# Optimization experiments

Hardware: AMD Instinct MI355X
Metric: run time of the kernel (lower is better)

## Reference

```python
import jax, jax.numpy as jnp
import numpy as np

DECAY = 0.99
EPS = 1e-05


def setup_inputs() -> dict:
    key = jax.random.key(0)
    k1, k2, k3 = jax.random.split(key, 3)
    N, K, D = 131072, 1024, 64
    return {
        "z": jax.random.normal(k1, (N, D), dtype=jnp.float32),
        "embeddings": jax.random.normal(k2, (K, D), dtype=jnp.float32),
        "cluster_size": jnp.ones((K,), dtype=jnp.float32),
        "ema_embed_sum": jax.random.normal(k3, (K, D), dtype=jnp.float32),
    }


def reference(z, embeddings, cluster_size, ema_embed_sum):
    # z: [N, D]; embeddings/ema_embed_sum: [K, D]; cluster_size: [K]
    N, D = z.shape
    K = embeddings.shape[0]

    # squared pairwise distances via the ||a||^2 - 2ab + ||b||^2 expansion
    d = (
        jnp.sum(z * z, axis=-1, keepdims=True)
        - 2.0 * (z @ embeddings.T)
        + jnp.sum(embeddings * embeddings, axis=-1)
    )  # [N, K]
    encoding_indices = jnp.argmin(d, axis=1)  # [N]
    z_q = embeddings[encoding_indices]  # [N, D]

    # EMA codebook update (training mode; one_hot.sum(0) == counts, one_hot.T @ z == segment_sum)
    counts = jax.ops.segment_sum(jnp.ones((N,), z.dtype), encoding_indices, num_segments=K)
    new_cluster_size = cluster_size * DECAY + (1.0 - DECAY) * counts
    embed_sum = jax.ops.segment_sum(z, encoding_indices, num_segments=K)  # [K, D]
    new_ema_embed_sum = ema_embed_sum * DECAY + (1.0 - DECAY) * embed_sum
    n = jnp.sum(new_cluster_size)
    cs = (new_cluster_size + EPS) / (n + K * EPS) * n
    new_embeddings = new_ema_embed_sum / cs[:, None]

    commitment_loss = jnp.mean((z - z_q) ** 2)
    z_q_st = z + jax.lax.stop_gradient(z_q - z)  # value == z_q
    return (z_q_st, commitment_loss, encoding_indices, new_embeddings, new_cluster_size, new_ema_embed_sum)
```

## Files before the change

kernel.cpp:

```cpp
#include <hip/hip_runtime.h>

#define N_PTS 131072
#define K_CODES 1024
#define DIM 64
#define DECAYF 0.99f
#define OMDF 0.01f
#define EPSF 1e-5f

#define OUT_ZQ      0
#define OUT_LOSS    8388608
#define OUT_IDX     8388609
#define OUT_NEWEMB  8519681
#define OUT_NEWCS   8585217
#define OUT_NEWEMA  8586241

#define WS_C8       0
#define WS_ACNT     8192
#define WS_LOSS     8208
#define WS_EMBSUM   8224
#define WS_ZERO_END 73760
#define WS_ENORM    73760
#define WS_CUR8     74784
#define WS_CS       82976
#define WS_AMBIG    84000
#define WS_ORDER    215072
#define WS_E2       346144

typedef __attribute__((ext_vector_type(8))) short bf16x8;
typedef __attribute__((ext_vector_type(4))) float f32x4;

static __device__ inline short f2bf(float f) {
    unsigned u = __float_as_uint(f);
    unsigned r = (u + 0x7fffu + ((u >> 16) & 1u)) >> 16;
    return (short)r;
}
static __device__ inline float bf2f(short h) {
    return __uint_as_float(((unsigned)(unsigned short)h) << 16);
}

__global__ __launch_bounds__(256) void econv_kernel(const float* __restrict__ E,
                                                    short* __restrict__ E2,
                                                    float* __restrict__ enorm) {
    int k = blockIdx.x * 256 + threadIdx.x;
    const float* ep = E + (size_t)k * DIM;
    short* o = E2 + (size_t)k * 128;
    float s = 0.f;
#pragma unroll
    for (int d = 0; d < 64; ++d) {
        float f = ep[d];
        s += f * f;
        float m = -2.f * f;
        short h = f2bf(m);
        o[d] = h;
        o[64 + d] = f2bf(m - bf2f(h));
    }
    enorm[k] = s;
}

__global__ __launch_bounds__(256) void argmin_mfma(const float* __restrict__ z,
                                                   const short* __restrict__ E2,
                                                   const float* __restrict__ enorm,
                                                   float* __restrict__ out_idx_f,
                                                   float* __restrict__ counts8,
                                                   int* __restrict__ ambig_cnt,
                                                   int* __restrict__ ambig,
                                                   float* __restrict__ loss_ws) {
    int tid = threadIdx.x;
    int w = tid >> 6, lane = tid & 63;
    int c = lane & 15, q = lane >> 4;
    int mbase = blockIdx.x * 256 + w * 64;

    bf16x8 a[4][4];
    float znorm_t[4];
#pragma unroll
    for (int t = 0; t < 4; ++t) {
        const float* zp = z + (size_t)(mbase + t * 16 + c) * DIM;
        const float4* z4a = (const float4*)(zp + q * 8);
        const float4* z4b = (const float4*)(zp + 32 + q * 8);
        float f[16];
        float4 v0 = z4a[0], v1 = z4a[1], v2 = z4b[0], v3 = z4b[1];
        f[0]=v0.x; f[1]=v0.y; f[2]=v0.z; f[3]=v0.w;
        f[4]=v1.x; f[5]=v1.y; f[6]=v1.z; f[7]=v1.w;
        f[8]=v2.x; f[9]=v2.y; f[10]=v2.z; f[11]=v2.w;
        f[12]=v3.x; f[13]=v3.y; f[14]=v3.z; f[15]=v3.w;
        float zn = 0.f;
#pragma unroll
        for (int j = 0; j < 16; ++j) zn += f[j] * f[j];
#pragma unroll
        for (int off = 16; off < 64; off <<= 1) zn += __shfl_xor(zn, off);
        znorm_t[t] = zn;
#pragma unroll
        for (int j = 0; j < 8; ++j) {
            short h0 = f2bf(f[j]);
            a[t][0][j] = h0;
            a[t][2][j] = f2bf(f[j] - bf2f(h0));
            short h1 = f2bf(f[8 + j]);
            a[t][1][j] = h1;
            a[t][3][j] = f2bf(f[8 + j] - bf2f(h1));
        }
    }

    float s1[16], s2[16];
#pragma unroll
    for (int idx = 0; idx < 16; ++idx) { s1[idx] = INFINITY; s2[idx] = INFINITY; }

    unsigned vcode = (unsigned)c;
    for (int tile = 0; tile < 64; ++tile) {
        const bf16x8* bp = (const bf16x8*)E2 + ((size_t)(tile * 16 + c) * 16) + q;
        bf16x8 bh0 = bp[0], bh1 = bp[4], bl0 = bp[8], bl1 = bp[12];
        float en = enorm[tile * 16 + c];
#pragma unroll
        for (int t = 0; t < 4; ++t) {
            f32x4 acc = {en, en, en, en};
            acc = __builtin_amdgcn_mfma_f32_16x16x32_bf16(a[t][0], bl0, acc, 0, 0, 0);
            acc = __builtin_amdgcn_mfma_f32_16x16x32_bf16(a[t][1], bl1, acc, 0, 0, 0);
            acc = __builtin_amdgcn_mfma_f32_16x16x32_bf16(a[t][2], bh0, acc, 0, 0, 0);
            acc = __builtin_amdgcn_mfma_f32_16x16x32_bf16(a[t][3], bh1, acc, 0, 0, 0);
            acc = __builtin_amdgcn_mfma_f32_16x16x32_bf16(a[t][0], bh0, acc, 0, 0, 0);
            acc = __builtin_amdgcn_mfma_f32_16x16x32_bf16(a[t][1], bh1, acc, 0, 0, 0);
#pragma unroll
            for (int i = 0; i < 4; ++i) {
                float sp = __uint_as_float(
                    (__float_as_uint(acc[i]) & 0xFFFFFC00u) | vcode);
                int idx = t * 4 + i;
                float ns2 = __builtin_amdgcn_fmed3f(s1[idx], s2[idx], sp);
                s1[idx] = fminf(s1[idx], sp);
                s2[idx] = ns2;
            }
        }
        vcode += 16;
    }

#pragma unroll
    for (int off = 1; off < 16; off <<= 1) {
#pragma unroll
        for (int idx = 0; idx < 16; ++idx) {
            float os1 = __shfl_xor(s1[idx], off);
            float os2 = __shfl_xor(s2[idx], off);
            float ns1 = fminf(s1[idx], os1);
            s2[idx] = fminf(fmaxf(s1[idx], os1), fminf(s2[idx], os2));
            s1[idx] = ns1;
        }
    }

    float znr[16];
#pragma unroll
    for (int t = 0; t < 4; ++t)
#pragma unroll
        for (int i = 0; i < 4; ++i)
            znr[t * 4 + i] = __shfl(znorm_t[t], (q << 4) | (q * 4 + i), 64);

    __shared__ float lred[16];
    float lsum = 0.f;
    if (c == 0) {
#pragma unroll
        for (int idx = 0; idx < 16; ++idx) {
            int t = idx >> 2, i = idx & 3;
            int row = mbase + t * 16 + q * 4 + i;
            unsigned b1 = __float_as_uint(s1[idx]);
            int code = (int)(b1 & 1023u);
            out_idx_f[row] = (float)code;
            float s1v = __uint_as_float(b1 & 0xFFFFFC00u);
            float gap = s2[idx] - s1[idx];
            float tau = 0.008f + 8e-4f * (fabsf(s1[idx]) + fabsf(s2[idx]));
            if (gap >= tau) {
                atomicAdd(&counts8[(((unsigned)row >> 8) & 7) * K_CODES + code], 1.0f);
                lsum += znr[idx] + s1v;
            } else {
                int p = atomicAdd(ambig_cnt, 1);
                ambig[p] = row;
            }
        }
        lred[w * 4 + q] = lsum;
    }
    __syncthreads();
    if (tid == 0) {
        float tot = 0.f;
#pragma unroll
        for (int i = 0; i < 16; ++i) tot += lred[i];
        atomicAdd(loss_ws, tot);
    }
}

__global__ __launch_bounds__(256) void rescue_kernel(const float* __restrict__ z,
                                                     const float* __restrict__ E,
                                                     const float* __restrict__ enorm,
                                                     const int* __restrict__ ambig_cnt,
                                                     const int* __restrict__ ambig,
                                                     float* __restrict__ out_idx_f,
                                                     float* __restrict__ counts8,
                                                     float* __restrict__ loss_ws) {
    int lane = threadIdx.x & 63;
    int wave = (blockIdx.x * 256 + threadIdx.x) >> 6;
    int nw = gridDim.x * 4;
    int cnt = *ambig_cnt;
    for (int a = 2 * wave; a < cnt; a += 2 * nw) {
        int row0 = ambig[a];
        bool two = (a + 1) < cnt;
        int row1 = two ? ambig[a + 1] : row0;
        const float4* zp0 = (const float4*)(z + (size_t)row0 * DIM);
        const float4* zp1 = (const float4*)(z + (size_t)row1 * DIM);
        float4 zr0[16], zr1[16];
        float zn0 = 0.f, zn1 = 0.f;
#pragma unroll
        for (int i = 0; i < 16; ++i) {
            float4 u = zp0[i], v = zp1[i];
            zr0[i] = u; zr1[i] = v;
            zn0 += u.x * u.x + u.y * u.y + u.z * u.z + u.w * u.w;
            zn1 += v.x * v.x + v.y * v.y + v.z * v.z + v.w * v.w;
        }
        float best0 = INFINITY, best1 = INFINITY;
        int bi0 = 0, bi1 = 0;
        for (int j = 0; j < 16; ++j) {
            int code = j * 64 + lane;
            const float4* ep = (const float4*)(E + (size_t)code * DIM);
            float a0 = 0.f, a1 = 0.f, a2 = 0.f, a3 = 0.f;
            float c0 = 0.f, c1 = 0.f, c2 = 0.f, c3 = 0.f;
#pragma unroll
            for (int i = 0; i < 16; ++i) {
                float4 ev = ep[i];
                a0 += zr0[i].x * ev.x; a1 += zr0[i].y * ev.y;
                a2 += zr0[i].z * ev.z; a3 += zr0[i].w * ev.w;
                c0 += zr1[i].x * ev.x; c1 += zr1[i].y * ev.y;
                c2 += zr1[i].z * ev.z; c3 += zr1[i].w * ev.w;
            }
            float en = enorm[code];
            float s0 = en - 2.f * ((a0 + a1) + (a2 + a3));
            float s1 = en - 2.f * ((c0 + c1) + (c2 + c3));
            if (s0 < best0) { best0 = s0; bi0 = code; }
            if (s1 < best1) { best1 = s1; bi1 = code; }
        }
#pragma unroll
        for (int off = 1; off < 64; off <<= 1) {
            float ob = __shfl_xor(best0, off);
            int oi = __shfl_xor(bi0, off);
            if (ob < best0 || (ob == best0 && oi < bi0)) { best0 = ob; bi0 = oi; }
            float ob1 = __shfl_xor(best1, off);
            int oi1 = __shfl_xor(bi1, off);
            if (ob1 < best1 || (ob1 == best1 && oi1 < bi1)) { best1 = ob1; bi1 = oi1; }
        }
        if (lane == 0) {
            out_idx_f[row0] = (float)bi0;
            atomicAdd(&counts8[(((unsigned)row0 >> 8) & 7) * K_CODES + bi0], 1.0f);
            float ladd = zn0 + best0;
            if (two) {
                out_idx_f[row1] = (float)bi1;
                atomicAdd(&counts8[(((unsigned)row1 >> 8) & 7) * K_CODES + bi1], 1.0f);
                ladd += zn1 + best1;
            }
            atomicAdd(loss_ws, ladd);
        }
    }
}

__global__ __launch_bounds__(256) void zq_write_kernel(const float* __restrict__ E,
                                                       const float* __restrict__ idx_f,
                                                       float* __restrict__ zq) {
    __shared__ int s_k[256];
    int tid = threadIdx.x;
    int rbase = blockIdx.x * 256;
    s_k[tid] = (int)idx_f[rbase + tid];
    __syncthreads();
    size_t ebase = (size_t)rbase * DIM;
#pragma unroll 4
    for (int it = 0; it < 64; ++it) {
        int le = it * 256 + tid;
        int rl = le >> 6, d = le & 63;
        zq[ebase + le] = E[(size_t)s_k[rl] * DIM + d];
    }
}

__global__ __launch_bounds__(1024) void scan_kernel(const float* __restrict__ cluster_size,
                                                    const float* __restrict__ counts8,
                                                    float* __restrict__ ncs_out,
                                                    float* __restrict__ cs_ws,
                                                    int* __restrict__ cursor8) {
    int k = threadIdx.x;
    int lane = k & 63, wv = k >> 6;
    float c8[8];
    float cnt = 0.f;
#pragma unroll
    for (int s = 0; s < 8; ++s) { c8[s] = counts8[s * K_CODES + k]; cnt += c8[s]; }
    float ncs = cluster_size[k] * DECAYF + OMDF * cnt;
    ncs_out[k] = ncs;

    int v = (int)cnt;
    int vs = v;
#pragma unroll
    for (int off = 1; off < 64; off <<= 1) {
        int o = __shfl_up(vs, off, 64);
        if (lane >= off) vs += o;
    }
    float fs = ncs;
#pragma unroll
    for (int off = 1; off < 64; off <<= 1) fs += __shfl_xor(fs, off);

    __shared__ int wtot[16];
    __shared__ float ftot[16];
    __shared__ float nsh;
    if (lane == 63) wtot[wv] = vs;
    if (lane == 0) ftot[wv] = fs;
    __syncthreads();
    if (k == 0) {
        int run = 0; float fn = 0.f;
#pragma unroll
        for (int i = 0; i < 16; ++i) {
            int t = wtot[i]; wtot[i] = run; run += t;
            fn += ftot[i];
        }
        nsh = fn;
    }
    __syncthreads();
    float n = nsh;
    cs_ws[k] = (ncs + EPSF) / (n + (float)K_CODES * EPSF) * n;

    int excl = vs - v + wtot[wv];
    int run = excl;
#pragma unroll
    for (int s = 0; s < 8; ++s) { cursor8[s * K_CODES + k] = run; run += (int)c8[s]; }
}

__global__ __launch_bounds__(256) void scatter_kernel(const float* __restrict__ idx_f,
                                                      int* __restrict__ cursor8,
                                                      int* __restrict__ order) {
    int row = blockIdx.x * 256 + threadIdx.x;
    int k = (int)idx_f[row];
    int shard = ((unsigned)row >> 8) & 7;
    int p = atomicAdd(&cursor8[shard * K_CODES + k], 1);
    order[p] = (k << 17) | row;
}

__global__ __launch_bounds__(256) void segsum_kernel(const float* __restrict__ z,
                                                     const int* __restrict__ order,
                                                     float* __restrict__ embsum) {
    int lane = threadIdx.x & 63;
    int w = threadIdx.x >> 6;
    int wave = blockIdx.x * 4 + w;
    int base = wave * 64;

    int my = order[base + lane];

    int cur = __shfl(my, 0, 64) >> 17;
    float sum = 0.f;
#pragma unroll 8
    for (int i = 0; i < 64; ++i) {
        int p = __shfl(my, i, 64);
        int row = p & 0x1FFFF;
        int code = p >> 17;
        float v = z[(size_t)row * DIM + lane];
        if (code != cur) {
            atomicAdd(&embsum[(size_t)cur * DIM + lane], sum);
            sum = 0.f;
            cur = code;
        }
        sum += v;
    }
    atomicAdd(&embsum[(size_t)cur * DIM + lane], sum);
}

__global__ __launch_bounds__(256) void ema2_kernel(const float* __restrict__ ema,
                                                   const float* __restrict__ embsum,
                                                   const float* __restrict__ cs_ws,
                                                   const float* __restrict__ loss_ws,
                                                   float* __restrict__ newema_out,
                                                   float* __restrict__ newemb_out,
                                                   float* __restrict__ loss_out) {
    int i = blockIdx.x * 256 + threadIdx.x;
    float nes = ema[i] * DECAYF + OMDF * embsum[i];
    newema_out[i] = nes;
    newemb_out[i] = nes / cs_ws[i >> 6];
    if (i == 0)
        loss_out[0] = loss_ws[0] * (1.0f / ((float)N_PTS * (float)DIM));
}

extern "C" void kernel_launch(void* const* d_in, const int* in_sizes, int n_in,
                              void* d_out, int out_size, void* d_ws, size_t ws_size,
                              hipStream_t stream) {
    const float* z            = (const float*)d_in[0];
    const float* E            = (const float*)d_in[1];
    const float* cluster_size = (const float*)d_in[2];
    const float* ema          = (const float*)d_in[3];
    float* out = (float*)d_out;
    float* ws  = (float*)d_ws;

    hipMemsetAsync(ws, 0, (size_t)WS_ZERO_END * sizeof(float), stream);

    econv_kernel<<<4, 256, 0, stream>>>(E, (short*)(ws + WS_E2), ws + WS_ENORM);

    argmin_mfma<<<N_PTS / 256, 256, 0, stream>>>(z, (const short*)(ws + WS_E2),
                                                 ws + WS_ENORM,
                                                 out + OUT_IDX,
                                                 ws + WS_C8,
                                                 (int*)(ws + WS_ACNT),
                                                 (int*)(ws + WS_AMBIG),
                                                 ws + WS_LOSS);

    rescue_kernel<<<512, 256, 0, stream>>>(z, E, ws + WS_ENORM,
                                           (const int*)(ws + WS_ACNT),
                                           (const int*)(ws + WS_AMBIG),
                                           out + OUT_IDX,
                                           ws + WS_C8,
                                           ws + WS_LOSS);

    zq_write_kernel<<<N_PTS / 256, 256, 0, stream>>>(E, out + OUT_IDX,
                                                     out + OUT_ZQ);

    scan_kernel<<<1, 1024, 0, stream>>>(cluster_size, ws + WS_C8,
                                        out + OUT_NEWCS, ws + WS_CS,
                                        (int*)(ws + WS_CUR8));

    scatter_kernel<<<N_PTS / 256, 256, 0, stream>>>(out + OUT_IDX,
                                                    (int*)(ws + WS_CUR8),
                                                    (int*)(ws + WS_ORDER));

    segsum_kernel<<<N_PTS / 256, 256, 0, stream>>>(z,
                                                   (const int*)(ws + WS_ORDER),
                                                   ws + WS_EMBSUM);

    ema2_kernel<<<K_CODES * DIM / 256, 256, 0, stream>>>(ema, ws + WS_EMBSUM,
                                                         ws + WS_CS,
                                                         ws + WS_LOSS,
                                                         out + OUT_NEWEMA,
                                                         out + OUT_NEWEMB,
                                                         out + OUT_LOSS);
}
```

Measured before the change: 249.2 us.

## Parallelize codebook conversion, halve argmin rows per block, fuse z_q write into scatter

The codebook conversion kernel now uses four threads per code with vectorized float4 loads and bf16x8 stores across 16 blocks, replacing 4 blocks where each thread serially handled one code. The argmin MFMA kernel processes 32 rows per wave instead of 64, doubling the grid, halving the register-resident A fragments and min trackers, and unrolling the tile loop by two. The z_q gather is merged into the scatter kernel, removing one launch and one re-read of the index array. The aim is more parallelism and occupancy at the cost of reading the codebook from L2 twice as often in argmin.

```diff
diff --git a/kernel.cpp b/kernel.cpp
--- a/kernel.cpp
+++ b/kernel.cpp
@@ -41,20 +41,35 @@
 __global__ __launch_bounds__(256) void econv_kernel(const float* __restrict__ E,
                                                     short* __restrict__ E2,
                                                     float* __restrict__ enorm) {
-    int k = blockIdx.x * 256 + threadIdx.x;
-    const float* ep = E + (size_t)k * DIM;
-    short* o = E2 + (size_t)k * 128;
+    int tid = threadIdx.x;
+    int code = blockIdx.x * 64 + (tid >> 2);
+    int seg = tid & 3;
+    const float4* e4 = (const float4*)(E + (size_t)code * DIM + seg * 16);
+    float4 v0 = e4[0], v1 = e4[1], v2 = e4[2], v3 = e4[3];
+    float f[16];
+    f[0]=v0.x; f[1]=v0.y; f[2]=v0.z; f[3]=v0.w;
+    f[4]=v1.x; f[5]=v1.y; f[6]=v1.z; f[7]=v1.w;
+    f[8]=v2.x; f[9]=v2.y; f[10]=v2.z; f[11]=v2.w;
+    f[12]=v3.x; f[13]=v3.y; f[14]=v3.z; f[15]=v3.w;
     float s = 0.f;
 #pragma unroll
-    for (int d = 0; d < 64; ++d) {
-        float f = ep[d];
-        s += f * f;
-        float m = -2.f * f;
+    for (int j = 0; j < 16; ++j) s += f[j] * f[j];
+    s += __shfl_xor(s, 1);
+    s += __shfl_xor(s, 2);
+    short hi[16], lo[16];
+#pragma unroll
+    for (int j = 0; j < 16; ++j) {
+        float m = -2.f * f[j];
         short h = f2bf(m);
-        o[d] = h;
-        o[64 + d] = f2bf(m - bf2f(h));
-    }
-    enorm[k] = s;
+        hi[j] = h;
+        lo[j] = f2bf(m - bf2f(h));
+    }
+    short* o = E2 + (size_t)code * 128 + seg * 16;
+    *(bf16x8*)(o)      = *(bf16x8*)(hi);
+    *(bf16x8*)(o + 8)  = *(bf16x8*)(hi + 8);
+    *(bf16x8*)(o + 64) = *(bf16x8*)(lo);
+    *(bf16x8*)(o + 72) = *(bf16x8*)(lo + 8);
+    if (seg == 0) enorm[code] = s;
 }
 
 __global__ __launch_bounds__(256) void argmin_mfma(const float* __restrict__ z,
@@ -68,12 +83,12 @@
     int tid = threadIdx.x;
     int w = tid >> 6, lane = tid & 63;
     int c = lane & 15, q = lane >> 4;
-    int mbase = blockIdx.x * 256 + w * 64;
-
-    bf16x8 a[4][4];
-    float znorm_t[4];
-#pragma unroll
-    for (int t = 0; t < 4; ++t) {
+    int mbase = blockIdx.x * 128 + w * 32;
+
+    bf16x8 a[2][4];
+    float znorm_t[2];
+#pragma unroll
+    for (int t = 0; t < 2; ++t) {
         const float* zp = z + (size_t)(mbase + t * 16 + c) * DIM;
         const float4* z4a = (const float4*)(zp + q * 8);
         const float4* z4b = (const float4*)(zp + 32 + q * 8);
@@ -100,17 +115,18 @@
         }
     }
 
-    float s1[16], s2[16];
-#pragma unroll
-    for (int idx = 0; idx < 16; ++idx) { s1[idx] = INFINITY; s2[idx] = INFINITY; }
+    float s1[8], s2[8];
+#pragma unroll
+    for (int idx = 0; idx < 8; ++idx) { s1[idx] = INFINITY; s2[idx] = INFINITY; }
 
     unsigned vcode = (unsigned)c;
+#pragma unroll 2
     for (int tile = 0; tile < 64; ++tile) {
         const bf16x8* bp = (const bf16x8*)E2 + ((size_t)(tile * 16 + c) * 16) + q;
         bf16x8 bh0 = bp[0], bh1 = bp[4], bl0 = bp[8], bl1 = bp[12];
         float en = enorm[tile * 16 + c];
 #pragma unroll
-        for (int t = 0; t < 4; ++t) {
+        for (int t = 0; t < 2; ++t) {
             f32x4 acc = {en, en, en, en};
             acc = __builtin_amdgcn_mfma_f32_16x16x32_bf16(a[t][0], bl0, acc, 0, 0, 0);
             acc = __builtin_amdgcn_mfma_f32_16x16x32_bf16(a[t][1], bl1, acc, 0, 0, 0);
@@ -134,7 +150,7 @@
 #pragma unroll
     for (int off = 1; off < 16; off <<= 1) {
 #pragma unroll
-        for (int idx = 0; idx < 16; ++idx) {
+        for (int idx = 0; idx < 8; ++idx) {
             float os1 = __shfl_xor(s1[idx], off);
             float os2 = __shfl_xor(s2[idx], off);
             float ns1 = fminf(s1[idx], os1);
@@ -143,9 +159,9 @@
         }
     }
 
-    float znr[16];
-#pragma unroll
-    for (int t = 0; t < 4; ++t)
+    float znr[8];
+#pragma unroll
+    for (int t = 0; t < 2; ++t)
 #pragma unroll
         for (int i = 0; i < 4; ++i)
             znr[t * 4 + i] = __shfl(znorm_t[t], (q << 4) | (q * 4 + i), 64);
@@ -154,7 +170,7 @@
     float lsum = 0.f;
     if (c == 0) {
 #pragma unroll
-        for (int idx = 0; idx < 16; ++idx) {
+        for (int idx = 0; idx < 8; ++idx) {
             int t = idx >> 2, i = idx & 3;
             int row = mbase + t * 16 + q * 4 + i;
             unsigned b1 = __float_as_uint(s1[idx]);
@@ -253,23 +269,6 @@
     }
 }
 
-__global__ __launch_bounds__(256) void zq_write_kernel(const float* __restrict__ E,
-                                                       const float* __restrict__ idx_f,
-                                                       float* __restrict__ zq) {
-    __shared__ int s_k[256];
-    int tid = threadIdx.x;
-    int rbase = blockIdx.x * 256;
-    s_k[tid] = (int)idx_f[rbase + tid];
-    __syncthreads();
-    size_t ebase = (size_t)rbase * DIM;
-#pragma unroll 4
-    for (int it = 0; it < 64; ++it) {
-        int le = it * 256 + tid;
-        int rl = le >> 6, d = le & 63;
-        zq[ebase + le] = E[(size_t)s_k[rl] * DIM + d];
-    }
-}
-
 __global__ __launch_bounds__(1024) void scan_kernel(const float* __restrict__ cluster_size,
                                                     const float* __restrict__ counts8,
                                                     float* __restrict__ ncs_out,
@@ -320,14 +319,28 @@
     for (int s = 0; s < 8; ++s) { cursor8[s * K_CODES + k] = run; run += (int)c8[s]; }
 }
 
-__global__ __launch_bounds__(256) void scatter_kernel(const float* __restrict__ idx_f,
-                                                      int* __restrict__ cursor8,
-                                                      int* __restrict__ order) {
-    int row = blockIdx.x * 256 + threadIdx.x;
+__global__ __launch_bounds__(256) void scatter_zq_kernel(const float* __restrict__ E,
+                                                         const float* __restrict__ idx_f,
+                                                         int* __restrict__ cursor8,
+                                                         int* __restrict__ order,
+                                                         float* __restrict__ zq) {
+    __shared__ int s_k[256];
+    int tid = threadIdx.x;
+    int rbase = blockIdx.x * 256;
+    int row = rbase + tid;
     int k = (int)idx_f[row];
+    s_k[tid] = k;
     int shard = ((unsigned)row >> 8) & 7;
     int p = atomicAdd(&cursor8[shard * K_CODES + k], 1);
     order[p] = (k << 17) | row;
+    __syncthreads();
+    size_t ebase = (size_t)rbase * DIM;
+#pragma unroll 4
+    for (int it = 0; it < 64; ++it) {
+        int le = it * 256 + tid;
+        int rl = le >> 6, d = le & 63;
+        zq[ebase + le] = E[(size_t)s_k[rl] * DIM + d];
+    }
 }
 
 __global__ __launch_bounds__(256) void segsum_kernel(const float* __restrict__ z,
@@ -385,9 +398,9 @@
 
     hipMemsetAsync(ws, 0, (size_t)WS_ZERO_END * sizeof(float), stream);
 
-    econv_kernel<<<4, 256, 0, stream>>>(E, (short*)(ws + WS_E2), ws + WS_ENORM);
-
-    argmin_mfma<<<N_PTS / 256, 256, 0, stream>>>(z, (const short*)(ws + WS_E2),
+    econv_kernel<<<K_CODES / 64, 256, 0, stream>>>(E, (short*)(ws + WS_E2), ws + WS_ENORM);
+
+    argmin_mfma<<<N_PTS / 128, 256, 0, stream>>>(z, (const short*)(ws + WS_E2),
                                                  ws + WS_ENORM,
                                                  out + OUT_IDX,
                                                  ws + WS_C8,
@@ -402,16 +415,14 @@
                                            ws + WS_C8,
                                            ws + WS_LOSS);
 
-    zq_write_kernel<<<N_PTS / 256, 256, 0, stream>>>(E, out + OUT_IDX,
-                                                     out + OUT_ZQ);
-
     scan_kernel<<<1, 1024, 0, stream>>>(cluster_size, ws + WS_C8,
                                         out + OUT_NEWCS, ws + WS_CS,
                                         (int*)(ws + WS_CUR8));
 
-    scatter_kernel<<<N_PTS / 256, 256, 0, stream>>>(out + OUT_IDX,
-                                                    (int*)(ws + WS_CUR8),
-                                                    (int*)(ws + WS_ORDER));
+    scatter_zq_kernel<<<N_PTS / 256, 256, 0, stream>>>(E, out + OUT_IDX,
+                                                       (int*)(ws + WS_CUR8),
+                                                       (int*)(ws + WS_ORDER),
+                                                       out + OUT_ZQ);
 
     segsum_kernel<<<N_PTS / 256, 256, 0, stream>>>(z,
                                                    (const int*)(ws + WS_ORDER),
```

Result: slower. 297.0 us (+19.1%).
